# Kernel optimization log

Measured on AMD Instinct MI355X. Metric: run time of the kernel, lower is better.

The kernel has to match this reference:

```python
import jax, jax.numpy as jnp
import numpy as np

B, S, D = 4, 1024, 1024
H, G = 16, 8            # num_heads, num_query_groups
HD = D // H             # head_dim = 64
E, TOPK, ED = 8, 2, 2 * D   # experts, top_k, expert_dim
GH = D // 2             # gate hidden
EPS = 1e-5


def setup_inputs() -> dict:
    key = jax.random.key(0)
    ks = iter(jax.random.split(key, 32))
    rn = lambda shape, s=0.02: jax.random.normal(next(ks), shape, jnp.float32) * s
    return {
        "x": jax.random.normal(next(ks), (B, S, D), jnp.float32),
        # GQA projections (stored [in, out])
        "wq": rn((D, G * HD)), "bq": jnp.zeros((G * HD,), jnp.float32),
        "wk": rn((D, D)), "bk": jnp.zeros((D,), jnp.float32),
        "wv": rn((D, D)), "bv": jnp.zeros((D,), jnp.float32),
        "wo": rn((D, D)), "bo": jnp.zeros((D,), jnp.float32),
        # LayerNorms
        "ln1_g": jnp.ones((D,), jnp.float32), "ln1_b": jnp.zeros((D,), jnp.float32),
        "ln2_g": jnp.ones((D,), jnp.float32), "ln2_b": jnp.zeros((D,), jnp.float32),
        # MoE gate: Linear(D, D//2) -> ReLU -> Linear(D//2, E)
        "gw1": rn((D, GH)), "gb1": jnp.zeros((GH,), jnp.float32),
        "gw2": rn((GH, E)), "gb2": jnp.zeros((E,), jnp.float32),
        # stacked expert FFNs: Linear(D, ED) -> GELU -> Linear(ED, D)
        "ew1": rn((E, D, ED)), "eb1": jnp.zeros((E, ED), jnp.float32),
        "ew2": rn((E, ED, D)), "eb2": jnp.zeros((E, D), jnp.float32),
    }


def _layernorm(x, g, b):
    mu = jnp.mean(x, axis=-1, keepdims=True)
    var = jnp.var(x, axis=-1, keepdims=True)
    return (x - mu) * jax.lax.rsqrt(var + EPS) * g + b


def _block(x, wq, bq, wk, bk, wv, bv, wo, bo, ln1_g, ln1_b, ln2_g, ln2_b,
           gw1, gb1, gw2, gb2, ew1, eb1, ew2, eb2):
    # --- GQA self-attention (dropout is identity in eval) ---
    h = _layernorm(x, ln1_g, ln1_b)
    q = (h @ wq + bq).reshape(B, S, G, HD).transpose(0, 2, 1, 3)   # [B,G,S,hd]
    k = (h @ wk + bk).reshape(B, S, H, HD).transpose(0, 2, 1, 3)   # [B,H,S,hd]
    v = (h @ wv + bv).reshape(B, S, H, HD).transpose(0, 2, 1, 3)
    q = jnp.repeat(q, H // G, axis=1)                              # repeat_interleave -> [B,H,S,hd]
    scores = jnp.einsum("bhqd,bhkd->bhqk", q, k) * (HD ** -0.5)
    attn = jax.nn.softmax(scores, axis=-1)
    ao = jnp.einsum("bhqk,bhkd->bhqd", attn, v)
    ao = ao.transpose(0, 2, 1, 3).reshape(B, S, D) @ wo + bo
    x = x + ao

    # --- MoE FFN ---
    h2 = _layernorm(x, ln2_g, ln2_b).reshape(-1, D)                # [T,D], T=B*S
    gate_logits = jax.nn.relu(h2 @ gw1 + gb1) @ gw2 + gb2          # [T,E]
    gate_w = jax.nn.softmax(gate_logits, axis=-1)
    top_w, top_i = jax.lax.top_k(gate_w, TOPK)                     # [T,k]
    top_w = jax.nn.softmax(top_w, axis=-1)                         # renormalize among top-k
    combine = jnp.sum(jax.nn.one_hot(top_i, E, dtype=h2.dtype) * top_w[..., None], axis=1)  # [T,E]
    hid = jax.nn.gelu(jnp.einsum("td,edh->teh", h2, ew1) + eb1, approximate=False)          # [T,E,ED]
    expert_out = jnp.einsum("teh,ehd->ted", hid, ew2) + eb2        # [T,E,D]
    moe = jnp.einsum("ted,te->td", expert_out, combine).reshape(B, S, D)
    return x + moe


def reference(x, wq, bq, wk, bk, wv, bv, wo, bo, ln1_g, ln1_b, ln2_g, ln2_b,
              gw1, gb1, gw2, gb2, ew1, eb1, ew2, eb2):
    return _block(x, wq, bq, wk, bk, wv, bv, wo, bo, ln1_g, ln1_b, ln2_g, ln2_b,
                  gw1, gb1, gw2, gb2, ew1, eb1, ew2, eb2)
```

## Files before the change

### kernel.cpp

```cpp
#include <hip/hip_runtime.h>

typedef __bf16 bf16x8 __attribute__((ext_vector_type(8)));
typedef float f32x4 __attribute__((ext_vector_type(4)));
typedef unsigned int u32x4 __attribute__((ext_vector_type(4)));
typedef unsigned int u32x2 __attribute__((ext_vector_type(2)));

#define DEV static __device__ __forceinline__

DEV unsigned short f2bf(float f) {
  unsigned int u = __builtin_bit_cast(unsigned int, f);
  u += 0x7fffu + ((u >> 16) & 1u);
  return (unsigned short)(u >> 16);
}
DEV float bf2f(unsigned int hbits) { return __builtin_bit_cast(float, hbits << 16); }
DEV unsigned pack2bf(float a, float b) {
  unsigned short x = __builtin_bit_cast(unsigned short, (__bf16)a);
  unsigned short y = __builtin_bit_cast(unsigned short, (__bf16)b);
  return (unsigned)x | ((unsigned)y << 16);
}

DEV bf16x8 load_bf8(const unsigned short* p) {
  u32x4 u = *(const u32x4*)p;
  return __builtin_bit_cast(bf16x8, u);
}
DEV void unpack8(u32x4 u, float f[8]) {
  f[0] = bf2f(u.x & 0xffffu); f[1] = bf2f(u.x >> 16);
  f[2] = bf2f(u.y & 0xffffu); f[3] = bf2f(u.y >> 16);
  f[4] = bf2f(u.z & 0xffffu); f[5] = bf2f(u.z >> 16);
  f[6] = bf2f(u.w & 0xffffu); f[7] = bf2f(u.w >> 16);
}
DEV void gload_lds16(const void* g, void* l) {
  __builtin_amdgcn_global_load_lds((const __attribute__((address_space(1))) void*)g,
                                   (__attribute__((address_space(3))) void*)l, 16, 0, 0);
}
DEV f32x4 mfma16(bf16x8 a, bf16x8 b, f32x4 c) {
  return __builtin_amdgcn_mfma_f32_16x16x32_bf16(a, b, c, 0, 0, 0);
}

__global__ __launch_bounds__(256) void cm_transpose(
    const float* __restrict__ src, unsigned short* __restrict__ dst,
    int K, int N, long srcStrideE, long dstStrideE) {
  src += (long)blockIdx.z * srcStrideE;
  dst += (long)blockIdx.z * dstStrideE;
  __shared__ float t[32][33];
  const int n0 = blockIdx.x * 32, k0 = blockIdx.y * 32;
  const int tx = threadIdx.x & 31, ty = threadIdx.x >> 5;
#pragma unroll
  for (int j = 0; j < 4; ++j) {
    int k = k0 + ty + j * 8, n = n0 + tx;
    if (k < K && n < N) t[ty + j * 8][tx] = src[(long)k * N + n];
  }
  __syncthreads();
#pragma unroll
  for (int j = 0; j < 4; ++j) {
    int n = n0 + ty + j * 8, k = k0 + tx;
    if (n < N && k < K) dst[(long)n * K + k] = f2bf(t[tx][ty + j * 8]);
  }
}

__global__ __launch_bounds__(256) void cm_transpose_split(
    const float* __restrict__ src, unsigned short* __restrict__ dhi,
    unsigned short* __restrict__ dlo, int K, int N) {
  __shared__ float t[32][33];
  const int n0 = blockIdx.x * 32, k0 = blockIdx.y * 32;
  const int tx = threadIdx.x & 31, ty = threadIdx.x >> 5;
#pragma unroll
  for (int j = 0; j < 4; ++j) {
    int k = k0 + ty + j * 8, n = n0 + tx;
    if (k < K && n < N) t[ty + j * 8][tx] = src[(long)k * N + n];
  }
  __syncthreads();
#pragma unroll
  for (int j = 0; j < 4; ++j) {
    int n = n0 + ty + j * 8, k = k0 + tx;
    if (n < N && k < K) {
      float v = t[tx][ty + j * 8];
      unsigned short hi = f2bf(v);
      dhi[(long)n * K + k] = hi;
      dlo[(long)n * K + k] = f2bf(v - bf2f(hi));
    }
  }
}

template <bool WLO>
__global__ __launch_bounds__(256) void cm_ln(
    const float* __restrict__ x, const float* __restrict__ g, const float* __restrict__ b,
    unsigned short* __restrict__ ob, unsigned short* __restrict__ olo) {
  const int row = blockIdx.x, tid = threadIdx.x;
  const f32x4 v = *(const f32x4*)(x + (long)row * 1024 + tid * 4);
  float s1 = v[0] + v[1] + v[2] + v[3];
  float s2 = v[0] * v[0] + v[1] * v[1] + v[2] * v[2] + v[3] * v[3];
#pragma unroll
  for (int m = 32; m >= 1; m >>= 1) { s1 += __shfl_xor(s1, m); s2 += __shfl_xor(s2, m); }
  __shared__ float r1[4], r2[4];
  if ((tid & 63) == 0) { r1[tid >> 6] = s1; r2[tid >> 6] = s2; }
  __syncthreads();
  s1 = r1[0] + r1[1] + r1[2] + r1[3];
  s2 = r2[0] + r2[1] + r2[2] + r2[3];
  const float mean = s1 * (1.f / 1024.f);
  const float rs = rsqrtf(s2 * (1.f / 1024.f) - mean * mean + 1e-5f);
  const f32x4 gg = *(const f32x4*)(g + tid * 4);
  const f32x4 bb = *(const f32x4*)(b + tid * 4);
  float o[4];
  unsigned short hi[4];
#pragma unroll
  for (int i = 0; i < 4; ++i) {
    o[i] = (v[i] - mean) * rs * gg[i] + bb[i];
    hi[i] = f2bf(o[i]);
  }
  u32x2 pk;
  pk.x = (unsigned)hi[0] | ((unsigned)hi[1] << 16);
  pk.y = (unsigned)hi[2] | ((unsigned)hi[3] << 16);
  *(u32x2*)(ob + (long)row * 1024 + tid * 4) = pk;
  if (WLO) {
    u32x2 pl;
    pl.x = (unsigned)f2bf(o[0] - bf2f(hi[0])) | ((unsigned)f2bf(o[1] - bf2f(hi[1])) << 16);
    pl.y = (unsigned)f2bf(o[2] - bf2f(hi[2])) | ((unsigned)f2bf(o[3] - bf2f(hi[3])) << 16);
    *(u32x2*)(olo + (long)row * 1024 + tid * 4) = pl;
  }
}

enum { EP_BF16 = 0, EP_RELU = 1, EP_GELU = 2, EP_RES_F32 = 3 };

template <int EPI, int MODE>
__global__ __launch_bounds__(256, 2) void cm_gemm_bt(
    const unsigned short* __restrict__ A, int lda,
    const unsigned short* __restrict__ BT, long btStrideE, int ldb,
    const float* __restrict__ bias, int biasStrideE,
    const float* __restrict__ res,
    void* __restrict__ outp, int ldc,
    int M, int K,
    const int* __restrict__ cnt, const int* __restrict__ offs,
    const int* __restrict__ rowidx) {
  int bx, by, z;
  if (MODE == 0) {
    const int gx = gridDim.x, gy = gridDim.y;
    const int nwg = gx * gy;
    int flat = (int)blockIdx.x + gx * (int)blockIdx.y;
    const int q = nwg >> 3, r = nwg & 7, xcd = flat & 7, idx = flat >> 3;
    flat = (xcd < r ? xcd * (q + 1) : r * (q + 1) + (xcd - r) * q) + idx;
    bx = flat % gx; by = flat / gx; z = 0;
  } else {
    bx = blockIdx.x; by = blockIdx.y; z = blockIdx.z;
  }

  int valid = M, rowbase = 0;
  const unsigned short* Bp = BT;
  const float* biasp = bias;
  if (MODE > 0) {
    valid = cnt[z];
    if (by * 128 >= valid) return;
    rowbase = offs[z];
    Bp += (long)z * btStrideE;
    biasp += (long)z * biasStrideE;
  }
  const int tid = threadIdx.x;
  const int brow = by * 128, bcol = bx * 128;
  const int wid = tid >> 6, lane = tid & 63;
  const int wr = wid >> 1, wc = wid & 1;

  const int srow = tid >> 3, sc = tid & 7;
  const int scg = ((sc ^ (srow & 7)) << 3);
  const int ldst = srow * 64 + sc * 8;

  __shared__ __align__(16) unsigned short As[128 * 64];
  __shared__ __align__(16) unsigned short Bs[128 * 64];

  long asrc[4], bsrc[4];
#pragma unroll
  for (int i = 0; i < 4; ++i) {
    int m = brow + srow + i * 32;
    if (MODE == 0) {
      asrc[i] = (long)m * lda;
    } else {
      int p = m < valid ? m : valid - 1;
      if (MODE == 1) asrc[i] = (long)rowidx[z * 4096 + p] * lda;
      else           asrc[i] = (long)(rowbase + p) * lda;
    }
    bsrc[i] = (long)(bcol + srow + i * 32) * ldb;
  }

  f32x4 acc[4][4] = {};

  for (int k0 = 0; k0 < K; k0 += 64) {
#pragma unroll
    for (int i = 0; i < 4; ++i) {
      gload_lds16(A + asrc[i] + k0 + scg, &As[ldst + i * 2048]);
      gload_lds16(Bp + bsrc[i] + k0 + scg, &Bs[ldst + i * 2048]);
    }
    __syncthreads();
#pragma unroll
    for (int ks = 0; ks < 2; ++ks) {
      bf16x8 af[4], bfr[4];
#pragma unroll
      for (int m = 0; m < 4; ++m) {
        const int r = wr * 64 + m * 16 + (lane & 15);
        af[m] = load_bf8(&As[r * 64 + (((ks * 4 + (lane >> 4)) ^ (lane & 7)) << 3)]);
      }
#pragma unroll
      for (int n = 0; n < 4; ++n) {
        const int r = wc * 64 + n * 16 + (lane & 15);
        bfr[n] = load_bf8(&Bs[r * 64 + (((ks * 4 + (lane >> 4)) ^ (lane & 7)) << 3)]);
      }
#pragma unroll
      for (int m = 0; m < 4; ++m)
#pragma unroll
        for (int n = 0; n < 4; ++n)
          acc[m][n] = mfma16(af[m], bfr[n], acc[m][n]);
    }
    __syncthreads();
  }

#pragma unroll
  for (int m = 0; m < 4; ++m) {
#pragma unroll
    for (int rr = 0; rr < 4; ++rr) {
      const int lrow = brow + wr * 64 + m * 16 + (lane >> 4) * 4 + rr;
      if (MODE > 0 && lrow >= valid) continue;
      const long orow = (long)(rowbase + lrow);
#pragma unroll
      for (int n = 0; n < 4; ++n) {
        const int gcol = bcol + wc * 64 + n * 16 + (lane & 15);
        float vv = acc[m][n][rr] + biasp[gcol];
        if constexpr (EPI == EP_RELU) vv = fmaxf(vv, 0.f);
        if constexpr (EPI == EP_GELU) vv = 0.5f * vv * (1.f + erff(vv * 0.70710678f));
        if constexpr (EPI == EP_RES_F32)
          ((float*)outp)[orow * ldc + gcol] = vv + res[orow * ldc + gcol];
        else
          ((unsigned short*)outp)[orow * ldc + gcol] = f2bf(vv);
      }
    }
  }
}

__global__ __launch_bounds__(256, 2) void cm_gemm_gate(
    const unsigned short* __restrict__ Ah, const unsigned short* __restrict__ Al,
    const unsigned short* __restrict__ Bh, const unsigned short* __restrict__ Bl,
    const float* __restrict__ bias, float* __restrict__ C) {
  const int tid = threadIdx.x;
  const int brow = blockIdx.y * 128, bcol = blockIdx.x * 128;
  const int wid = tid >> 6, lane = tid & 63;
  const int wr = wid >> 1, wc = wid & 1;
  const int srow0 = tid >> 2, scol = (tid & 3) * 8;

  __shared__ __align__(16) unsigned short Ash[128 * 32], Asl[128 * 32];
  __shared__ __align__(16) unsigned short Bsh[128 * 32], Bsl[128 * 32];

  f32x4 acc[4][4] = {};

  for (int k0 = 0; k0 < 1024; k0 += 32) {
#pragma unroll
    for (int i = 0; i < 2; ++i) {
      const long ar = (long)(brow + srow0 + i * 64) * 1024 + k0 + scol;
      const long br = (long)(bcol + srow0 + i * 64) * 1024 + k0 + scol;
      const int lo = (srow0 + i * 64) * 32 + scol;
      gload_lds16(Ah + ar, &Ash[lo]);
      gload_lds16(Al + ar, &Asl[lo]);
      gload_lds16(Bh + br, &Bsh[lo]);
      gload_lds16(Bl + br, &Bsl[lo]);
    }
    __syncthreads();
    bf16x8 ah[4], al[4], bh[4], bl[4];
#pragma unroll
    for (int m = 0; m < 4; ++m) {
      const int ro = (wr * 64 + m * 16 + (lane & 15)) * 32 + (lane >> 4) * 8;
      ah[m] = load_bf8(&Ash[ro]); al[m] = load_bf8(&Asl[ro]);
    }
#pragma unroll
    for (int n = 0; n < 4; ++n) {
      const int ro = (wc * 64 + n * 16 + (lane & 15)) * 32 + (lane >> 4) * 8;
      bh[n] = load_bf8(&Bsh[ro]); bl[n] = load_bf8(&Bsl[ro]);
    }
#pragma unroll
    for (int m = 0; m < 4; ++m)
#pragma unroll
      for (int n = 0; n < 4; ++n) {
        acc[m][n] = mfma16(al[m], bh[n], acc[m][n]);
        acc[m][n] = mfma16(ah[m], bl[n], acc[m][n]);
        acc[m][n] = mfma16(ah[m], bh[n], acc[m][n]);
      }
    __syncthreads();
  }

#pragma unroll
  for (int m = 0; m < 4; ++m)
#pragma unroll
    for (int rr = 0; rr < 4; ++rr) {
      const long orow = brow + wr * 64 + m * 16 + (lane >> 4) * 4 + rr;
#pragma unroll
      for (int n = 0; n < 4; ++n) {
        const int gcol = bcol + wc * 64 + n * 16 + (lane & 15);
        C[orow * 512 + gcol] = fmaxf(acc[m][n][rr] + bias[gcol], 0.f);
      }
    }
}

__global__ __launch_bounds__(256) void cm_vtrans(
    const unsigned short* __restrict__ qkv, unsigned short* __restrict__ Vt) {
  const int stile = blockIdx.x, bh = blockIdx.y;
  const int b = bh >> 4, h = bh & 15;
  const int tid = threadIdx.x;
  __shared__ __align__(16) unsigned short t[64][72];
  const int d0 = (tid & 7) * 8, sl = tid >> 3;
#pragma unroll
  for (int i = 0; i < 2; ++i) {
    const int s = sl + i * 32;
    *(u32x4*)&t[s][d0] =
        *(const u32x4*)(qkv + (long)(b * 1024 + stile * 64 + s) * 2560 + 1536 + h * 64 + d0);
  }
  __syncthreads();
  const int s0 = (tid & 7) * 8, dl = tid >> 3;
#pragma unroll
  for (int i = 0; i < 2; ++i) {
    const int d = dl + i * 32;
    unsigned short vals[8];
#pragma unroll
    for (int j = 0; j < 8; ++j) vals[j] = t[s0 + j][d];
    u32x4 u;
    u.x = vals[0] | ((unsigned)vals[1] << 16);
    u.y = vals[2] | ((unsigned)vals[3] << 16);
    u.z = vals[4] | ((unsigned)vals[5] << 16);
    u.w = vals[6] | ((unsigned)vals[7] << 16);
    *(u32x4*)(Vt + (long)(bh * 64 + d) * 1024 + stile * 64 + s0) = u;
  }
}

__global__ __launch_bounds__(256, 2) void cm_attn(
    const unsigned short* __restrict__ qkv,
    const unsigned short* __restrict__ Vt,
    unsigned short* __restrict__ ao) {
  int flat = (int)blockIdx.x;
  flat = (flat & 7) * 256 + (flat >> 3);
  const int qt = flat & 31, bh = flat >> 5;
  const int b = bh >> 4, h = bh & 15, g = h >> 1;
  const int tid = threadIdx.x, wid = tid >> 6, lane = tid & 63;
  const int q0 = qt * 32;

  __shared__ __align__(16) unsigned short sc[32][1028];
  __shared__ float rowrcp[32];

  bf16x8 bq[2][2];
#pragma unroll
  for (int nf = 0; nf < 2; ++nf)
#pragma unroll
    for (int ks = 0; ks < 2; ++ks)
      bq[nf][ks] = load_bf8(qkv + (long)(b * 1024 + q0 + nf * 16 + (lane & 15)) * 2560 +
                            g * 64 + ks * 32 + (lane >> 4) * 8);

#pragma unroll 2
  for (int c = 0; c < 4; ++c) {
    const int kb = wid * 256 + c * 64;
    f32x4 acc[4][2] = {};
#pragma unroll
    for (int ks = 0; ks < 2; ++ks) {
      bf16x8 ak[4];
#pragma unroll
      for (int mf = 0; mf < 4; ++mf)
        ak[mf] = load_bf8(qkv + (long)(b * 1024 + kb + mf * 16 + (lane & 15)) * 2560 +
                          512 + h * 64 + ks * 32 + (lane >> 4) * 8);
#pragma unroll
      for (int mf = 0; mf < 4; ++mf)
#pragma unroll
        for (int nf = 0; nf < 2; ++nf)
          acc[mf][nf] = mfma16(ak[mf], bq[nf][ks], acc[mf][nf]);
    }
#pragma unroll
    for (int mf = 0; mf < 4; ++mf)
#pragma unroll
      for (int nf = 0; nf < 2; ++nf) {
        const int q = nf * 16 + (lane & 15);
        const int key = kb + mf * 16 + (lane >> 4) * 4;
        u32x2 pk;
        pk.x = pack2bf(__expf(acc[mf][nf][0] * 0.125f), __expf(acc[mf][nf][1] * 0.125f));
        pk.y = pack2bf(__expf(acc[mf][nf][2] * 0.125f), __expf(acc[mf][nf][3] * 0.125f));
        *(u32x2*)&sc[q][key] = pk;
      }
  }
  __syncthreads();

  {
    const int row = tid >> 3, seg = tid & 7;
    float sum = 0.f;
#pragma unroll
    for (int i = 0; i < 16; ++i) {
      float f[8];
      unpack8(*(const u32x4*)&sc[row][i * 64 + seg * 8], f);
#pragma unroll
      for (int j = 0; j < 8; ++j) sum += f[j];
    }
#pragma unroll
    for (int m = 4; m >= 1; m >>= 1) sum += __shfl_xor(sum, m);
    if (seg == 0) rowrcp[row] = 1.f / sum;
  }
  __syncthreads();

  {
    f32x4 acc[2] = {};
    const unsigned short* vtb = Vt + (long)bh * 64 * 1024;
#pragma unroll 4
    for (int k0 = 0; k0 < 1024; k0 += 32) {
      const bf16x8 bv =
          load_bf8(vtb + (long)(wid * 16 + (lane & 15)) * 1024 + k0 + (lane >> 4) * 8);
#pragma unroll
      for (int m = 0; m < 2; ++m) {
        const bf16x8 ap = load_bf8(&sc[m * 16 + (lane & 15)][k0 + (lane >> 4) * 8]);
        acc[m] = mfma16(ap, bv, acc[m]);
      }
    }
#pragma unroll
    for (int m = 0; m < 2; ++m)
#pragma unroll
      for (int rr = 0; rr < 4; ++rr) {
        const int q = m * 16 + (lane >> 4) * 4 + rr;
        const int d = wid * 16 + (lane & 15);
        ao[(long)(b * 1024 + q0 + q) * 1024 + h * 64 + d] = f2bf(acc[m][rr] * rowrcp[q]);
      }
  }
}

__global__ __launch_bounds__(64) void cm_route_pick(
    const float* __restrict__ g1f, const float* __restrict__ gw2, const float* __restrict__ gb2,
    int* __restrict__ pick, int* __restrict__ slot_e, float* __restrict__ rwt) {
  const int t = blockIdx.x, lane = threadIdx.x;
  f32x4 a0 = *(const f32x4*)(g1f + (long)t * 512 + lane * 8);
  f32x4 a1 = *(const f32x4*)(g1f + (long)t * 512 + lane * 8 + 4);
  float logit[8];
#pragma unroll
  for (int e = 0; e < 8; ++e) {
    float s = 0.f;
#pragma unroll
    for (int j = 0; j < 4; ++j) {
      s += a0[j] * gw2[(lane * 8 + j) * 8 + e];
      s += a1[j] * gw2[(lane * 8 + 4 + j) * 8 + e];
    }
#pragma unroll
    for (int m = 32; m >= 1; m >>= 1) s += __shfl_xor(s, m);
    logit[e] = s + gb2[e];
  }
  float mx = logit[0];
#pragma unroll
  for (int e = 1; e < 8; ++e) mx = fmaxf(mx, logit[e]);
  float p[8], sum = 0.f;
#pragma unroll
  for (int e = 0; e < 8; ++e) { p[e] = __expf(logit[e] - mx); sum += p[e]; }
  const float rs = 1.f / sum;
#pragma unroll
  for (int e = 0; e < 8; ++e) p[e] *= rs;
  int i0 = 0;
#pragma unroll
  for (int e = 1; e < 8; ++e) if (p[e] > p[i0]) i0 = e;
  int i1 = (i0 == 0) ? 1 : 0;
#pragma unroll
  for (int e = 0; e < 8; ++e) if (e != i0 && p[e] > p[i1]) i1 = e;
  const float w0 = 1.f / (1.f + __expf(p[i1] - p[i0]));
  if (lane == 0) {
    pick[t] = i0 | (i1 << 8);
    slot_e[t * 2] = i0; slot_e[t * 2 + 1] = i1;
    rwt[t * 2] = w0;    rwt[t * 2 + 1] = 1.f - w0;
  }
}

__global__ __launch_bounds__(256) void cm_route_place(
    const int* __restrict__ pick, int* __restrict__ cnt,
    int* __restrict__ etok, int* __restrict__ slot_p) {
  const int t = blockIdx.x * 256 + threadIdx.x;
  const int lane = threadIdx.x & 63;
  const int pk = pick[t];
  const int p0 = pk & 15, p1 = (pk >> 8) & 15;
  const unsigned long long lt = ((unsigned long long)1 << lane) - 1;
  int my_r0 = 0, my_c0p1 = 0, my_r1 = 0, tot = 0;
#pragma unroll
  for (int e = 0; e < 8; ++e) {
    const unsigned long long m0 = __ballot(p0 == e);
    const unsigned long long m1 = __ballot(p1 == e);
    if (p0 == e) my_r0 = __popcll(m0 & lt);
    if (p1 == e) { my_c0p1 = __popcll(m0); my_r1 = __popcll(m1 & lt); }
    if (lane == e) tot = __popcll(m0) + __popcll(m1);
  }
  int base = 0;
  if (lane < 8 && tot > 0) base = atomicAdd(&cnt[lane], tot);
  const int b0 = __shfl(base, p0);
  const int b1 = __shfl(base, p1);
  const int pos0 = b0 + my_r0;
  const int pos1 = b1 + my_c0p1 + my_r1;
  etok[p0 * 4096 + pos0] = t;
  etok[p1 * 4096 + pos1] = t;
  slot_p[t * 2] = pos0;
  slot_p[t * 2 + 1] = pos1;
}

__global__ void cm_offs(const int* __restrict__ cnt, int* __restrict__ offs) {
  if (threadIdx.x == 0) {
    int s = 0;
#pragma unroll
    for (int e = 0; e < 8; ++e) { offs[e] = s; s += cnt[e]; }
  }
}

__global__ __launch_bounds__(256) void cm_combine(
    const float* __restrict__ x2, const unsigned short* __restrict__ eo,
    const int* __restrict__ slot_e, const int* __restrict__ slot_p,
    const float* __restrict__ rwt, const int* __restrict__ offs,
    float* __restrict__ outp) {
  const int t = blockIdx.x, tid = threadIdx.x;
  const long r0 = (long)(offs[slot_e[t * 2]] + slot_p[t * 2]);
  const long r1 = (long)(offs[slot_e[t * 2 + 1]] + slot_p[t * 2 + 1]);
  const float w0 = rwt[t * 2], w1 = rwt[t * 2 + 1];
  const f32x4 xv = *(const f32x4*)(x2 + (long)t * 1024 + tid * 4);
  u32x2 u0 = *(const u32x2*)(eo + r0 * 1024 + tid * 4);
  u32x2 u1 = *(const u32x2*)(eo + r1 * 1024 + tid * 4);
  f32x4 o;
  o[0] = xv[0] + w0 * bf2f(u0.x & 0xffffu) + w1 * bf2f(u1.x & 0xffffu);
  o[1] = xv[1] + w0 * bf2f(u0.x >> 16) + w1 * bf2f(u1.x >> 16);
  o[2] = xv[2] + w0 * bf2f(u0.y & 0xffffu) + w1 * bf2f(u1.y & 0xffffu);
  o[3] = xv[3] + w0 * bf2f(u0.y >> 16) + w1 * bf2f(u1.y >> 16);
  *(f32x4*)(outp + (long)t * 1024 + tid * 4) = o;
}

extern "C" void kernel_launch(void* const* d_in, const int* in_sizes, int n_in,
                              void* d_out, int out_size, void* d_ws, size_t ws_size,
                              hipStream_t stream) {
  if (n_in < 21) return;
  const float* x    = (const float*)d_in[0];
  const float* wq   = (const float*)d_in[1];
  const float* bq   = (const float*)d_in[2];
  const float* wk   = (const float*)d_in[3];
  const float* bk   = (const float*)d_in[4];
  const float* wv   = (const float*)d_in[5];
  const float* bv   = (const float*)d_in[6];
  const float* wo   = (const float*)d_in[7];
  const float* bo   = (const float*)d_in[8];
  const float* ln1g = (const float*)d_in[9];
  const float* ln1b = (const float*)d_in[10];
  const float* ln2g = (const float*)d_in[11];
  const float* ln2b = (const float*)d_in[12];
  const float* gw1  = (const float*)d_in[13];
  const float* gb1  = (const float*)d_in[14];
  const float* gw2  = (const float*)d_in[15];
  const float* gb2  = (const float*)d_in[16];
  const float* ew1  = (const float*)d_in[17];
  const float* eb1  = (const float*)d_in[18];
  const float* ew2  = (const float*)d_in[19];
  const float* eb2  = (const float*)d_in[20];
  float* outp = (float*)d_out;

  char* ws = (char*)d_ws;
  size_t off = 0;
  auto carve = [&](size_t bytes) -> char* {
    char* p = ws + off;
    off += (bytes + 255) & ~(size_t)255;
    return p;
  };
  unsigned short* wqkvT = (unsigned short*)carve(2560l * 1024 * 2);
  unsigned short* woT   = (unsigned short*)carve(1024l * 1024 * 2);
  unsigned short* gw1hT = (unsigned short*)carve(512l * 1024 * 2);
  unsigned short* gw1lT = (unsigned short*)carve(512l * 1024 * 2);
  unsigned short* ew1T  = (unsigned short*)carve(8l * 2048 * 1024 * 2);
  unsigned short* ew2T  = (unsigned short*)carve(8l * 1024 * 2048 * 2);
  float* bqkv           = (float*)carve(2560 * 4);
  unsigned short* hbuf  = (unsigned short*)carve(4096l * 1024 * 2);
  unsigned short* qkvl  = (unsigned short*)carve(4096l * 2560 * 2);
  unsigned short* Vt    = (unsigned short*)carve(4096l * 1024 * 2);
  unsigned short* ao    = (unsigned short*)carve(4096l * 1024 * 2);
  unsigned short* h2    = (unsigned short*)carve(4096l * 1024 * 2);
  unsigned short* h2lo  = (unsigned short*)carve(4096l * 1024 * 2);
  int* cnt              = (int*)carve(8 * 4);
  int* offs             = (int*)carve(8 * 4);
  int* etok             = (int*)carve(8l * 4096 * 4);
  int* slot_e           = (int*)carve(8192 * 4);
  int* slot_p           = (int*)carve(8192 * 4);
  float* rwt            = (float*)carve(8192 * 4);
  int* pick             = (int*)carve(4096 * 4);
  unsigned short* hid   = (unsigned short*)carve(8192l * 2048 * 2);
  unsigned short* eo    = (unsigned short*)carve(8192l * 1024 * 2);
  if (off > ws_size) return;
  float* x2 = outp;
  float* g1f = (float*)Vt;

  (void)hipMemsetAsync(cnt, 0, 8 * 4, stream);
  (void)hipMemcpyAsync(bqkv, (const void*)bq, 512 * 4, hipMemcpyDeviceToDevice, stream);
  (void)hipMemcpyAsync(bqkv + 512, (const void*)bk, 1024 * 4, hipMemcpyDeviceToDevice, stream);
  (void)hipMemcpyAsync(bqkv + 1536, (const void*)bv, 1024 * 4, hipMemcpyDeviceToDevice, stream);

  cm_transpose<<<dim3(16, 32, 1), 256, 0, stream>>>(wq, wqkvT, 1024, 512, 0l, 0l);
  cm_transpose<<<dim3(32, 32, 1), 256, 0, stream>>>(wk, wqkvT + 512l * 1024, 1024, 1024, 0l, 0l);
  cm_transpose<<<dim3(32, 32, 1), 256, 0, stream>>>(wv, wqkvT + 1536l * 1024, 1024, 1024, 0l, 0l);
  cm_transpose<<<dim3(32, 32, 1), 256, 0, stream>>>(wo, woT, 1024, 1024, 0l, 0l);
  cm_transpose_split<<<dim3(16, 32, 1), 256, 0, stream>>>(gw1, gw1hT, gw1lT, 1024, 512);
  cm_transpose<<<dim3(64, 32, 8), 256, 0, stream>>>(ew1, ew1T, 1024, 2048, 1024l * 2048, 2048l * 1024);
  cm_transpose<<<dim3(32, 64, 8), 256, 0, stream>>>(ew2, ew2T, 2048, 1024, 2048l * 1024, 1024l * 2048);

  cm_ln<false><<<4096, 256, 0, stream>>>(x, ln1g, ln1b, hbuf, nullptr);
  cm_gemm_bt<EP_BF16, 0><<<dim3(20, 32, 1), 256, 0, stream>>>(
      hbuf, 1024, wqkvT, 0l, 1024, bqkv, 0, nullptr, qkvl, 2560, 4096, 1024,
      nullptr, nullptr, nullptr);
  cm_vtrans<<<dim3(16, 64, 1), 256, 0, stream>>>(qkvl, Vt);
  cm_attn<<<dim3(2048, 1, 1), 256, 0, stream>>>(qkvl, Vt, ao);
  cm_gemm_bt<EP_RES_F32, 0><<<dim3(8, 32, 1), 256, 0, stream>>>(
      ao, 1024, woT, 0l, 1024, bo, 0, x, x2, 1024, 4096, 1024,
      nullptr, nullptr, nullptr);
  cm_ln<true><<<4096, 256, 0, stream>>>(x2, ln2g, ln2b, h2, h2lo);

  cm_gemm_gate<<<dim3(4, 32, 1), 256, 0, stream>>>(h2, h2lo, gw1hT, gw1lT, gb1, g1f);
  cm_route_pick<<<4096, 64, 0, stream>>>(g1f, gw2, gb2, pick, slot_e, rwt);
  cm_route_place<<<16, 256, 0, stream>>>(pick, cnt, etok, slot_p);
  cm_offs<<<1, 64, 0, stream>>>(cnt, offs);

  cm_gemm_bt<EP_GELU, 1><<<dim3(16, 32, 8), 256, 0, stream>>>(
      h2, 1024, ew1T, 2048l * 1024, 1024, eb1, 2048, nullptr, hid, 2048, 4096, 1024,
      cnt, offs, etok);
  cm_gemm_bt<EP_BF16, 2><<<dim3(8, 32, 8), 256, 0, stream>>>(
      hid, 2048, ew2T, 1024l * 2048, 2048, eb2, 1024, nullptr, eo, 1024, 4096, 2048,
      cnt, offs, nullptr);
  cm_combine<<<4096, 256, 0, stream>>>(x2, eo, slot_e, slot_p, rwt, offs, outp);
}
```

Measured before the change: 458.7 us.

## Stream attention over key chunks to shrink shared-memory score buffer

The attention kernel now processes keys in four 256-key rounds. Each round computes exp-scores into a small shared tile and immediately accumulates P·V, instead of materialising the full 32x1024 score row in shared memory. Row sums are accumulated in registers during the exp pass and reduced at the end, which drops the separate sum pass. The smaller LDS footprint lets launch bounds ask for 4 blocks per CU, raising occupancy, at the cost of two extra barriers per round and less overlap inside each block.

Result: faster. 445.1 us (-3.0%).

```diff
diff --git a/kernel.cpp b/kernel.cpp
--- a/kernel.cpp
+++ b/kernel.cpp
@@ -325,7 +325,7 @@
   }
 }
 
-__global__ __launch_bounds__(256, 2) void cm_attn(
+__global__ __launch_bounds__(256, 4) void cm_attn(
     const unsigned short* __restrict__ qkv,
     const unsigned short* __restrict__ Vt,
     unsigned short* __restrict__ ao) {
@@ -336,7 +336,8 @@
   const int tid = threadIdx.x, wid = tid >> 6, lane = tid & 63;
   const int q0 = qt * 32;
 
-  __shared__ __align__(16) unsigned short sc[32][1028];
+  __shared__ __align__(16) unsigned short sc[32][260];
+  __shared__ float rsum[4][32];
   __shared__ float rowrcp[32];
 
   bf16x8 bq[2][2];
@@ -347,75 +348,78 @@
       bq[nf][ks] = load_bf8(qkv + (long)(b * 1024 + q0 + nf * 16 + (lane & 15)) * 2560 +
                             g * 64 + ks * 32 + (lane >> 4) * 8);
 
-#pragma unroll 2
-  for (int c = 0; c < 4; ++c) {
-    const int kb = wid * 256 + c * 64;
-    f32x4 acc[4][2] = {};
-#pragma unroll
-    for (int ks = 0; ks < 2; ++ks) {
-      bf16x8 ak[4];
+  f32x4 oacc[2] = {};
+  float ps[2] = {0.f, 0.f};
+  const unsigned short* vtb = Vt + (long)bh * 64 * 1024;
+
+#pragma unroll 1
+  for (int rnd = 0; rnd < 4; ++rnd) {
+    {
+      const int kb = rnd * 256 + wid * 64;
+      f32x4 acc[4][2] = {};
+#pragma unroll
+      for (int ks = 0; ks < 2; ++ks) {
+        bf16x8 ak[4];
+#pragma unroll
+        for (int mf = 0; mf < 4; ++mf)
+          ak[mf] = load_bf8(qkv + (long)(b * 1024 + kb + mf * 16 + (lane & 15)) * 2560 +
+                            512 + h * 64 + ks * 32 + (lane >> 4) * 8);
+#pragma unroll
+        for (int mf = 0; mf < 4; ++mf)
+#pragma unroll
+          for (int nf = 0; nf < 2; ++nf)
+            acc[mf][nf] = mfma16(ak[mf], bq[nf][ks], acc[mf][nf]);
+      }
 #pragma unroll
       for (int mf = 0; mf < 4; ++mf)
-        ak[mf] = load_bf8(qkv + (long)(b * 1024 + kb + mf * 16 + (lane & 15)) * 2560 +
-                          512 + h * 64 + ks * 32 + (lane >> 4) * 8);
-#pragma unroll
-      for (int mf = 0; mf < 4; ++mf)
-#pragma unroll
-        for (int nf = 0; nf < 2; ++nf)
-          acc[mf][nf] = mfma16(ak[mf], bq[nf][ks], acc[mf][nf]);
-    }
-#pragma unroll
-    for (int mf = 0; mf < 4; ++mf)
-#pragma unroll
-      for (int nf = 0; nf < 2; ++nf) {
-        const int q = nf * 16 + (lane & 15);
-        const int key = kb + mf * 16 + (lane >> 4) * 4;
-        u32x2 pk;
-        pk.x = pack2bf(__expf(acc[mf][nf][0] * 0.125f), __expf(acc[mf][nf][1] * 0.125f));
-        pk.y = pack2bf(__expf(acc[mf][nf][2] * 0.125f), __expf(acc[mf][nf][3] * 0.125f));
-        *(u32x2*)&sc[q][key] = pk;
-      }
-  }
-  __syncthreads();
-
-  {
-    const int row = tid >> 3, seg = tid & 7;
-    float sum = 0.f;
-#pragma unroll
-    for (int i = 0; i < 16; ++i) {
-      float f[8];
-      unpack8(*(const u32x4*)&sc[row][i * 64 + seg * 8], f);
-#pragma unroll
-      for (int j = 0; j < 8; ++j) sum += f[j];
-    }
-#pragma unroll
-    for (int m = 4; m >= 1; m >>= 1) sum += __shfl_xor(sum, m);
-    if (seg == 0) rowrcp[row] = 1.f / sum;
-  }
-  __syncthreads();
-
-  {
-    f32x4 acc[2] = {};
-    const unsigned short* vtb = Vt + (long)bh * 64 * 1024;
-#pragma unroll 4
-    for (int k0 = 0; k0 < 1024; k0 += 32) {
-      const bf16x8 bv =
-          load_bf8(vtb + (long)(wid * 16 + (lane & 15)) * 1024 + k0 + (lane >> 4) * 8);
+#pragma unroll
+        for (int nf = 0; nf < 2; ++nf) {
+          const int q = nf * 16 + (lane & 15);
+          const int kl = wid * 64 + mf * 16 + (lane >> 4) * 4;
+          float e0 = __expf(acc[mf][nf][0] * 0.125f);
+          float e1 = __expf(acc[mf][nf][1] * 0.125f);
+          float e2 = __expf(acc[mf][nf][2] * 0.125f);
+          float e3 = __expf(acc[mf][nf][3] * 0.125f);
+          ps[nf] += (e0 + e1) + (e2 + e3);
+          u32x2 pk;
+          pk.x = pack2bf(e0, e1);
+          pk.y = pack2bf(e2, e3);
+          *(u32x2*)&sc[q][kl] = pk;
+        }
+    }
+    __syncthreads();
+#pragma unroll
+    for (int k0 = 0; k0 < 256; k0 += 32) {
+      const bf16x8 bv = load_bf8(vtb + (long)(wid * 16 + (lane & 15)) * 1024 +
+                                 rnd * 256 + k0 + (lane >> 4) * 8);
 #pragma unroll
       for (int m = 0; m < 2; ++m) {
         const bf16x8 ap = load_bf8(&sc[m * 16 + (lane & 15)][k0 + (lane >> 4) * 8]);
-        acc[m] = mfma16(ap, bv, acc[m]);
+        oacc[m] = mfma16(ap, bv, oacc[m]);
       }
     }
-#pragma unroll
-    for (int m = 0; m < 2; ++m)
-#pragma unroll
-      for (int rr = 0; rr < 4; ++rr) {
-        const int q = m * 16 + (lane >> 4) * 4 + rr;
-        const int d = wid * 16 + (lane & 15);
-        ao[(long)(b * 1024 + q0 + q) * 1024 + h * 64 + d] = f2bf(acc[m][rr] * rowrcp[q]);
-      }
-  }
+    __syncthreads();
+  }
+
+#pragma unroll
+  for (int m = 16; m <= 32; m <<= 1) {
+    ps[0] += __shfl_xor(ps[0], m);
+    ps[1] += __shfl_xor(ps[1], m);
+  }
+  if (lane < 16) { rsum[wid][lane] = ps[0]; rsum[wid][lane + 16] = ps[1]; }
+  __syncthreads();
+  if (tid < 32)
+    rowrcp[tid] = 1.f / (rsum[0][tid] + rsum[1][tid] + rsum[2][tid] + rsum[3][tid]);
+  __syncthreads();
+
+#pragma unroll
+  for (int m = 0; m < 2; ++m)
+#pragma unroll
+    for (int rr = 0; rr < 4; ++rr) {
+      const int q = m * 16 + (lane >> 4) * 4 + rr;
+      const int d = wid * 16 + (lane & 15);
+      ao[(long)(b * 1024 + q0 + q) * 1024 + h * 64 + d] = f2bf(oacc[m][rr] * rowrcp[q]);
+    }
 }
 
 __global__ __launch_bounds__(64) void cm_route_pick(
```
